# Performance work log

Hardware: AMD Instinct MI355X
Metric: run time of the kernel (lower is better)

The kernel has to match this reference:

```python
import jax, jax.numpy as jnp
import numpy as np

N = 8192   # number of points
C = 64     # feature channels (in_channels == out_channels in PointTrans_Layer)
K = 16     # KNNGraph(k=16)


def mlp2(h, w1, b1, gamma, beta, w2, b2):
    # PyG MLP(num_layers=2): Linear -> BatchNorm(eval: affine) -> ReLU -> Linear
    h = h @ w1 + b1
    h = gamma * h + beta          # BN in eval mode with running mean 0 / var 1
    h = jax.nn.relu(h)
    return h @ w2 + b2


def knn_indices(pos, k):
    # pairwise squared distances, self excluded (KNNGraph loop=False)
    sq = jnp.sum(pos * pos, axis=-1)                      # [N]
    d = sq[:, None] + sq[None, :] - 2.0 * (pos @ pos.T)   # [N, N]
    n = pos.shape[0]
    d = d.at[jnp.arange(n), jnp.arange(n)].set(jnp.inf)
    _, idx = jax.lax.top_k(-d, k)                         # [N, k] nearest neighbors
    return idx


def setup_inputs() -> dict:
    key = jax.random.key(0)
    ks = jax.random.split(key, 20)
    s = 1.0 / np.sqrt(C)
    inp = {
        "x": jax.random.normal(ks[0], (N, C), jnp.float32),
        "pos": jax.random.uniform(ks[1], (N, 3), jnp.float32) * 10.0,
        # PointTransformerConv linears
        "w_src": jax.random.normal(ks[2], (C, C), jnp.float32) * s,   # lin_src (no bias)
        "w_dst": jax.random.normal(ks[3], (C, C), jnp.float32) * s,   # lin_dst (no bias)
        "w_lin": jax.random.normal(ks[4], (C, C), jnp.float32) * s,   # lin (value)
        "b_lin": jnp.zeros((C,), jnp.float32),
        # pos_nn: MLP(3 -> C -> C)
        "p1w": jax.random.normal(ks[5], (3, C), jnp.float32) * (1.0 / np.sqrt(3)),
        "p1b": jnp.zeros((C,), jnp.float32),
        "p1g": jnp.ones((C,), jnp.float32),
        "p1bt": jnp.zeros((C,), jnp.float32),
        "p2w": jax.random.normal(ks[6], (C, C), jnp.float32) * s,
        "p2b": jnp.zeros((C,), jnp.float32),
        # attn_nn: MLP(C -> C -> C)
        "a1w": jax.random.normal(ks[7], (C, C), jnp.float32) * s,
        "a1b": jnp.zeros((C,), jnp.float32),
        "a1g": jnp.ones((C,), jnp.float32),
        "a1bt": jnp.zeros((C,), jnp.float32),
        "a2w": jax.random.normal(ks[8], (C, C), jnp.float32) * s,
        "a2b": jnp.zeros((C,), jnp.float32),
        # linear_up
        "uw": jax.random.normal(ks[9], (C, C), jnp.float32) * s,
        "ub": jnp.zeros((C,), jnp.float32),
    }
    return inp


def reference(x, pos, w_src, w_dst, w_lin, b_lin,
              p1w, p1b, p1g, p1bt, p2w, p2b,
              a1w, a1b, a1g, a1bt, a2w, a2b, uw, ub):
    idx = knn_indices(pos, K)                       # [N, K] neighbor (source) ids
    a_dst = x @ w_dst                               # alpha_i   [N, C]
    a_src = x @ w_src                               # alpha_j   [N, C]
    v = x @ w_lin + b_lin                           # values    [N, C]

    rel = pos[:, None, :] - pos[idx]                # pos_i - pos_j  [N, K, 3]
    delta = mlp2(rel, p1w, p1b, p1g, p1bt, p2w, p2b)            # [N, K, C]
    alpha = a_dst[:, None, :] - a_src[idx] + delta              # [N, K, C]
    alpha = mlp2(alpha, a1w, a1b, a1g, a1bt, a2w, a2b)          # [N, K, C]
    w = jax.nn.softmax(alpha, axis=1)               # softmax over incoming edges
    out = jnp.sum(w * (v[idx] + delta), axis=1)     # [N, C]

    out = out @ uw + ub                             # linear_up
    return out + x                                  # residual
```

## Files before the change

kernel.cpp:

```cpp
#include <hip/hip_runtime.h>
#include <math.h>

#define N 8192
#define C 64
#define K 16
#define NB 8
#define QB 8
#define LNODES 8
#define HS 72

typedef unsigned long long u64;
typedef unsigned int u32;

typedef float  f32x4v  __attribute__((ext_vector_type(4)));
typedef __bf16 bf16x8  __attribute__((ext_vector_type(8)));

__device__ __forceinline__ unsigned short bfr(float f) {
    u32 u = __float_as_uint(f);
    return (unsigned short)((u + 0x7fffu + ((u >> 16) & 1u)) >> 16);
}

__global__ __launch_bounds__(256) void prep_pos4(const float* __restrict__ pos,
                                                 float4* __restrict__ pos4) {
    int j = blockIdx.x * 256 + threadIdx.x;
    if (j < N) {
        const float px = pos[3*j], py = pos[3*j+1], pz = pos[3*j+2];
        pos4[j] = make_float4(px, py, pz, fmaf(px, px, fmaf(py, py, pz * pz)));
    }
}

__global__ __launch_bounds__(256) void prep_wT(const float* __restrict__ p2w,
                                               const float* __restrict__ a1w,
                                               const float* __restrict__ a2w,
                                               unsigned short* __restrict__ wT) {
    int t = blockIdx.x * 256 + threadIdx.x;
    if (t < 3 * C * C) {
        const int m = t >> 12, r = t & (C*C - 1);
        const int e = r >> 6, c = r & 63;
        const float* w = (m == 0) ? p2w : (m == 1) ? a1w : a2w;
        wT[m * C * HS + c * HS + e] = bfr(w[r]);
    }
}

__global__ __launch_bounds__(512) void knn_kernel(const float4* __restrict__ pos4,
                                                  int* __restrict__ idx_out) {
    __shared__ float          smin[QB][512];
    __shared__ float          sthr[QB];
    __shared__ unsigned short s_tl[QB][64];
    __shared__ int            s_tlc[QB];
    __shared__ int            s_buf[QB][96];
    __shared__ double         s_d[QB][96];
    __shared__ int            s_cnt[QB];
    __shared__ double         s_fd[QB][K];
    __shared__ int            s_fi[QB][K];

    const int tid  = threadIdx.x;
    const int w    = tid >> 6;
    const int lane = tid & 63;
    const int i0   = blockIdx.x * QB;

    if (tid < QB) { s_cnt[tid] = 0; s_tlc[tid] = 0; }

    float qx[QB], qy[QB], qz[QB];
    #pragma unroll
    for (int q = 0; q < QB; ++q) {
        const float4 p = pos4[i0 + q];
        qx[q] = p.x; qy[q] = p.y; qz[q] = p.z;
    }

    float mn[QB];
    #pragma unroll
    for (int q = 0; q < QB; ++q) mn[q] = INFINITY;
    #pragma unroll 4
    for (int s = 0; s < 16; ++s) {
        const int j = (s << 9) + tid;
        const float4 pj = pos4[j];
        #pragma unroll
        for (int q = 0; q < QB; ++q) {
            const float dot = fmaf(qx[q], pj.x, fmaf(qy[q], pj.y, qz[q] * pj.z));
            const float pr  = fmaf(-2.0f, dot, pj.w);
            mn[q] = fminf(mn[q], pr);
        }
    }
    #pragma unroll
    for (int q = 0; q < QB; ++q) smin[q][tid] = mn[q];
    __syncthreads();

    float thw;
    {
        float v[8];
        #pragma unroll
        for (int k = 0; k < 8; ++k) v[k] = smin[w][lane + 64*k];
        float ml = fminf(fminf(fminf(v[0], v[1]), fminf(v[2], v[3])),
                         fminf(fminf(v[4], v[5]), fminf(v[6], v[7])));
        float cur = ml, T = 0.0f;
        for (int r = 0; r < K + 1; ++r) {
            float m = cur;
            #pragma unroll
            for (int off = 32; off; off >>= 1) m = fminf(m, __shfl_xor(m, off, 64));
            T = m;
            cur = (cur == m) ? INFINITY : cur;
        }
        thw = T + 1e-3f + 4e-6f * fabsf(T);
        if (lane == 0) sthr[w] = thw;
        #pragma unroll
        for (int k = 0; k < 8; ++k) {
            if (v[k] <= thw) {
                const int slot = atomicAdd(&s_tlc[w], 1);
                if (slot < 64) s_tl[w][slot] = (unsigned short)(lane + 64*k);
            }
        }
    }

    {
        const int lc_raw = s_tlc[w];
        const int lc = lc_raw < 64 ? lc_raw : 64;
        const float qwx = qx[w], qwy = qy[w], qwz = qz[w];
        for (int p = lane; p < lc * 16; p += 64) {
            const int t = s_tl[w][p >> 4];
            const int s = p & 15;
            const int j = (s << 9) + t;
            const float4 pj = pos4[j];
            const float dot = fmaf(qwx, pj.x, fmaf(qwy, pj.y, qwz * pj.z));
            const float pr  = fmaf(-2.0f, dot, pj.w);
            if (pr <= thw) {
                const int slot = atomicAdd(&s_cnt[w], 1);
                if (slot < 96) s_buf[w][slot] = j;
            }
        }
    }

    {
        const int q  = w;
        const int iq = i0 + q;
        const int cno = s_cnt[q];
        if (cno <= 96 && s_tlc[q] <= 64) {
            const int cn = cno;
            const double dqx = (double)qx[q], dqy = (double)qy[q], dqz = (double)qz[q];
            for (int sl = lane; sl < cn; sl += 64) {
                const int jj = s_buf[q][sl];
                const float4 pj = pos4[jj];
                const double dx = dqx - (double)pj.x;
                const double dy = dqy - (double)pj.y;
                const double dz = dqz - (double)pj.z;
                s_d[q][sl] = dx*dx + dy*dy + dz*dz;
            }
            for (int sl = lane; sl < cn; sl += 64) {
                const int jj = s_buf[q][sl];
                if (jj == iq) continue;
                const double dj = s_d[q][sl];
                int r = 0;
                for (int e = 0; e < cn; ++e) {
                    const double de = s_d[q][e];
                    const int    je = s_buf[q][e];
                    r += (de < dj || (de == dj && je < jj)) ? 1 : 0;
                }
                const int selfb = (dj > 0.0 || (dj == 0.0 && iq < jj)) ? 1 : 0;
                const int rr = r - selfb;
                if (rr < K) idx_out[iq*K + rr] = jj;
            }
        } else {
            if (lane == 0) {
                for (int kk = 0; kk < K; ++kk) { s_fd[w][kk] = 1e300; s_fi[w][kk] = 0x7fffffff; }
                const double dqx = (double)qx[q], dqy = (double)qy[q], dqz = (double)qz[q];
                for (int j = 0; j < N; ++j) {
                    if (j == iq) continue;
                    const float4 pj = pos4[j];
                    const double dx = dqx - (double)pj.x;
                    const double dy = dqy - (double)pj.y;
                    const double dz = dqz - (double)pj.z;
                    const double dd = dx*dx + dy*dy + dz*dz;
                    if (dd < s_fd[w][K-1] || (dd == s_fd[w][K-1] && j < s_fi[w][K-1])) {
                        int p = K - 1;
                        while (p > 0 && (dd < s_fd[w][p-1] || (dd == s_fd[w][p-1] && j < s_fi[w][p-1]))) {
                            s_fd[w][p] = s_fd[w][p-1]; s_fi[w][p] = s_fi[w][p-1]; --p;
                        }
                        s_fd[w][p] = dd; s_fi[w][p] = j;
                    }
                }
                for (int kk = 0; kk < K; ++kk) idx_out[iq*K + kk] = s_fi[w][kk];
            }
        }
    }
}

__global__ __launch_bounds__(192) void lin3_kernel(const float* __restrict__ x,
    const float* __restrict__ w_src, const float* __restrict__ w_dst,
    const float* __restrict__ w_lin, const float* __restrict__ b_lin,
    float* __restrict__ a_dst, float* __restrict__ a_src, float* __restrict__ v) {
    __shared__ float xr[LNODES][C];
    const int n0  = blockIdx.x * LNODES;
    const int tid = threadIdx.x;
    const int cc  = tid & 63;
    const int m   = tid >> 6;

    const float* w = (m == 0) ? w_dst : (m == 1) ? w_src : w_lin;
    float wreg[C];
    #pragma unroll
    for (int k = 0; k < C; ++k) wreg[k] = w[k*C + cc];

    for (int t = tid; t < LNODES*C; t += 192) xr[t >> 6][t & 63] = x[n0*C + t];
    __syncthreads();

    const float binit = (m == 2) ? b_lin[cc] : 0.0f;
    float* o = (m == 0) ? a_dst : (m == 1) ? a_src : v;
    for (int nn = 0; nn < LNODES; ++nn) {
        float acc = binit;
        const float4* xv = (const float4*)xr[nn];
        #pragma unroll
        for (int k4 = 0; k4 < 16; ++k4) {
            const float4 xx = xv[k4];
            acc = fmaf(xx.x, wreg[4*k4+0], acc);
            acc = fmaf(xx.y, wreg[4*k4+1], acc);
            acc = fmaf(xx.z, wreg[4*k4+2], acc);
            acc = fmaf(xx.w, wreg[4*k4+3], acc);
        }
        o[(n0 + nn)*C + cc] = acc;
    }
}

__device__ __forceinline__ void mm16x64(const unsigned short* Hb, const unsigned short* wT,
                                        int c0, int sg, f32x4v acc[4]) {
    const bf16x8 a0 = *reinterpret_cast<const bf16x8*>(Hb + c0*HS + sg*8);
    const bf16x8 a1 = *reinterpret_cast<const bf16x8*>(Hb + c0*HS + 32 + sg*8);
    #pragma unroll
    for (int q = 0; q < 4; ++q) {
        const unsigned short* wr = wT + (q*16 + c0)*HS + sg*8;
        const bf16x8 b0 = *reinterpret_cast<const bf16x8*>(wr);
        const bf16x8 b1 = *reinterpret_cast<const bf16x8*>(wr + 32);
        acc[q] = __builtin_amdgcn_mfma_f32_16x16x32_bf16(a0, b0, acc[q], 0, 0, 0);
        acc[q] = __builtin_amdgcn_mfma_f32_16x16x32_bf16(a1, b1, acc[q], 0, 0, 0);
    }
}

__global__ __launch_bounds__(512, 4) void edge_kernel(
    const float* __restrict__ x, const float* __restrict__ pos,
    const int* __restrict__ nidx,
    const float* __restrict__ a_dst, const float* __restrict__ a_src, const float* __restrict__ v,
    const unsigned short* __restrict__ wTg,
    const float* __restrict__ p1w, const float* __restrict__ p1b,
    const float* __restrict__ p1g, const float* __restrict__ p1bt,
    const float* __restrict__ p2b,
    const float* __restrict__ a1b, const float* __restrict__ a1g, const float* __restrict__ a1bt,
    const float* __restrict__ a2b,
    const float* __restrict__ uw, const float* __restrict__ ub,
    float* __restrict__ out) {

    __shared__ __align__(16) unsigned short sWT[3 * C * HS];
    __shared__ __align__(16) float          uwf[C * C];
    __shared__ __align__(16) unsigned short sHb[NB * K * HS];
    __shared__ __align__(16) float4         sMisc4[NB * 16];
    __shared__ int                          sIdx[NB * K];

    const int tid  = threadIdx.x;
    const int w    = tid >> 6;
    const int lane = tid & 63;
    const int c0   = tid & 15;
    const int sg   = (tid >> 4) & 3;
    const int n    = blockIdx.x * NB + w;

    unsigned short* Hlb = sHb + w * (K * HS);
    float4*         Ml4 = sMisc4 + w * 16;
    float*          Mlf = (float*)Ml4;
    int*            Il  = sIdx + w * K;

    {
        const float4* s4 = (const float4*)wTg;
        float4* d4 = (float4*)sWT;
        #pragma unroll
        for (int q = 0; q < 4; ++q) {
            const int e = tid + q*512;
            if (e < 1728) d4[e] = s4[e];
        }
        float4* du = (float4*)uwf;
        const float4* su = (const float4*)uw;
        du[tid] = su[tid]; du[tid + 512] = su[tid + 512];
    }
    if (lane < K) {
        const int j = nidx[n*K + lane];
        Il[lane] = j;
        float4 r;
        r.x = pos[3*n]   - pos[3*j];
        r.y = pos[3*n+1] - pos[3*j+1];
        r.z = pos[3*n+2] - pos[3*j+2];
        r.w = 0.0f;
        Ml4[lane] = r;
    }
    __syncthreads();

    int c4[4];
    #pragma unroll
    for (int q = 0; q < 4; ++q) c4[q] = q*16 + c0;

    {
        float W0[4], W1[4], W2[4], B_[4], G_[4], BT[4];
        #pragma unroll
        for (int q = 0; q < 4; ++q) {
            const int cc = c4[q];
            W0[q] = p1w[cc]; W1[q] = p1w[C + cc]; W2[q] = p1w[2*C + cc];
            B_[q] = p1b[cc]; G_[q] = p1g[cc];     BT[q] = p1bt[cc];
        }
        #pragma unroll
        for (int r = 0; r < 4; ++r) {
            const float4 rr = Ml4[sg*4 + r];
            #pragma unroll
            for (int q = 0; q < 4; ++q) {
                float t = fmaf(rr.x, W0[q], fmaf(rr.y, W1[q], fmaf(rr.z, W2[q], B_[q])));
                t = fmaxf(fmaf(G_[q], t, BT[q]), 0.0f);
                Hlb[(sg*4 + r)*HS + c4[q]] = bfr(t);
            }
        }
    }

    f32x4v acc[4], del[4];
    #pragma unroll
    for (int q = 0; q < 4; ++q) { const float b_ = p2b[c4[q]]; acc[q] = (f32x4v){b_, b_, b_, b_}; }
    mm16x64(Hlb, sWT, c0, sg, acc);
    #pragma unroll
    for (int q = 0; q < 4; ++q) del[q] = acc[q];

    int jr[4];
    #pragma unroll
    for (int r = 0; r < 4; ++r) jr[r] = Il[sg*4 + r];
    float adstv[4];
    #pragma unroll
    for (int q = 0; q < 4; ++q) adstv[q] = a_dst[n*C + c4[q]];

    #pragma unroll
    for (int r = 0; r < 4; ++r) {
        #pragma unroll
        for (int q = 0; q < 4; ++q) {
            const float t = adstv[q] - a_src[jr[r]*C + c4[q]] + acc[q][r];
            Hlb[(sg*4 + r)*HS + c4[q]] = bfr(t);
        }
    }

    #pragma unroll
    for (int q = 0; q < 4; ++q) { const float b_ = a1b[c4[q]]; acc[q] = (f32x4v){b_, b_, b_, b_}; }
    mm16x64(Hlb, sWT + C*HS, c0, sg, acc);
    #pragma unroll
    for (int q = 0; q < 4; ++q) {
        const float g_ = a1g[c4[q]], bt_ = a1bt[c4[q]];
        #pragma unroll
        for (int r = 0; r < 4; ++r) {
            const float h2 = fmaxf(fmaf(g_, acc[q][r], bt_), 0.0f);
            Hlb[(sg*4 + r)*HS + c4[q]] = bfr(h2);
        }
    }

    #pragma unroll
    for (int q = 0; q < 4; ++q) { const float b_ = a2b[c4[q]]; acc[q] = (f32x4v){b_, b_, b_, b_}; }
    mm16x64(Hlb, sWT + 2*C*HS, c0, sg, acc);

    float o_[4];
    #pragma unroll
    for (int q = 0; q < 4; ++q) {
        float vgq[4];
        #pragma unroll
        for (int r = 0; r < 4; ++r) vgq[r] = v[jr[r]*C + c4[q]];
        float lm = fmaxf(fmaxf(acc[q][0], acc[q][1]), fmaxf(acc[q][2], acc[q][3]));
        lm = fmaxf(lm, __shfl_xor(lm, 16, 64));
        lm = fmaxf(lm, __shfl_xor(lm, 32, 64));
        float ls = 0.0f, lo = 0.0f;
        #pragma unroll
        for (int r = 0; r < 4; ++r) {
            const float e_ = __expf(acc[q][r] - lm);
            ls += e_;
            lo = fmaf(e_, vgq[r] + del[q][r], lo);
        }
        ls += __shfl_xor(ls, 16, 64); ls += __shfl_xor(ls, 32, 64);
        lo += __shfl_xor(lo, 16, 64); lo += __shfl_xor(lo, 32, 64);
        o_[q] = lo / ls;
    }
    if (sg == 0) {
        #pragma unroll
        for (int q = 0; q < 4; ++q) Mlf[c4[q]] = o_[q];
    }

    float facc = ub[lane] + x[n*C + lane];
    #pragma unroll 4
    for (int e4 = 0; e4 < 16; ++e4) {
        const float4 g4 = Ml4[e4];
        facc = fmaf(g4.x, uwf[(e4*4+0)*C + lane], facc);
        facc = fmaf(g4.y, uwf[(e4*4+1)*C + lane], facc);
        facc = fmaf(g4.z, uwf[(e4*4+2)*C + lane], facc);
        facc = fmaf(g4.w, uwf[(e4*4+3)*C + lane], facc);
    }
    out[n*C + lane] = facc;
}

extern "C" void kernel_launch(void* const* d_in, const int* in_sizes, int n_in,
                              void* d_out, int out_size, void* d_ws, size_t ws_size,
                              hipStream_t stream) {
    const float* x     = (const float*)d_in[0];
    const float* pos   = (const float*)d_in[1];
    const float* w_src = (const float*)d_in[2];
    const float* w_dst = (const float*)d_in[3];
    const float* w_lin = (const float*)d_in[4];
    const float* b_lin = (const float*)d_in[5];
    const float* p1w   = (const float*)d_in[6];
    const float* p1b   = (const float*)d_in[7];
    const float* p1g   = (const float*)d_in[8];
    const float* p1bt  = (const float*)d_in[9];
    const float* p2w   = (const float*)d_in[10];
    const float* p2b   = (const float*)d_in[11];
    const float* a1w   = (const float*)d_in[12];
    const float* a1b   = (const float*)d_in[13];
    const float* a1g   = (const float*)d_in[14];
    const float* a1bt  = (const float*)d_in[15];
    const float* a2w   = (const float*)d_in[16];
    const float* a2b   = (const float*)d_in[17];
    const float* uw    = (const float*)d_in[18];
    const float* ub    = (const float*)d_in[19];
    float* out = (float*)d_out;

    char* ws    = (char*)d_ws;
    int*    idx  = (int*)ws;
    float*  adst = (float*)(ws + (size_t)N*K*sizeof(int));
    float*  asrc = adst + (size_t)N*C;
    float*  vv   = asrc + (size_t)N*C;
    float4* pos4 = (float4*)(vv + (size_t)N*C);
    unsigned short* wTg = (unsigned short*)(pos4 + N);

    prep_pos4 <<<(N + 255)/256, 256, 0, stream>>>(pos, pos4);
    prep_wT   <<<(3*C*C + 255)/256, 256, 0, stream>>>(p2w, a1w, a2w, wTg);
    knn_kernel<<<N/QB, 512, 0, stream>>>(pos4, idx);
    lin3_kernel<<<N/LNODES, 192, 0, stream>>>(x, w_src, w_dst, w_lin, b_lin, adst, asrc, vv);
    edge_kernel<<<N/NB, 512, 0, stream>>>(x, pos, idx, adst, asrc, vv, wTg,
        p1w, p1b, p1g, p1bt, p2b, a1b, a1g, a1bt, a2b, uw, ub, out);
}
```

Baseline: 62.88 us.

## Fuse KNN into edge kernel and merge prep kernels into one launch

Merges the two prep kernels into a single launch and fuses the KNN search into the edge kernel. Neighbor indices now stay in shared memory, and the shared-memory areas of the two phases are overlaid with a union. This removes the global idx round trip and two kernel launches. The uw matrix is now read from global memory instead of being staged in LDS, which lowers LDS use and lets occupancy rise to 6 blocks. The cost is that KNN and edge work are serialized inside one block and can no longer overlap the way separate kernels did.

```diff
diff --git a/kernel.cpp b/kernel.cpp
--- a/kernel.cpp
+++ b/kernel.cpp
@@ -20,166 +20,23 @@
     return (unsigned short)((u + 0x7fffu + ((u >> 16) & 1u)) >> 16);
 }
 
-__global__ __launch_bounds__(256) void prep_pos4(const float* __restrict__ pos,
-                                                 float4* __restrict__ pos4) {
-    int j = blockIdx.x * 256 + threadIdx.x;
-    if (j < N) {
-        const float px = pos[3*j], py = pos[3*j+1], pz = pos[3*j+2];
-        pos4[j] = make_float4(px, py, pz, fmaf(px, px, fmaf(py, py, pz * pz)));
-    }
-}
-
-__global__ __launch_bounds__(256) void prep_wT(const float* __restrict__ p2w,
-                                               const float* __restrict__ a1w,
-                                               const float* __restrict__ a2w,
-                                               unsigned short* __restrict__ wT) {
-    int t = blockIdx.x * 256 + threadIdx.x;
-    if (t < 3 * C * C) {
-        const int m = t >> 12, r = t & (C*C - 1);
-        const int e = r >> 6, c = r & 63;
-        const float* w = (m == 0) ? p2w : (m == 1) ? a1w : a2w;
-        wT[m * C * HS + c * HS + e] = bfr(w[r]);
-    }
-}
-
-__global__ __launch_bounds__(512) void knn_kernel(const float4* __restrict__ pos4,
-                                                  int* __restrict__ idx_out) {
-    __shared__ float          smin[QB][512];
-    __shared__ float          sthr[QB];
-    __shared__ unsigned short s_tl[QB][64];
-    __shared__ int            s_tlc[QB];
-    __shared__ int            s_buf[QB][96];
-    __shared__ double         s_d[QB][96];
-    __shared__ int            s_cnt[QB];
-    __shared__ double         s_fd[QB][K];
-    __shared__ int            s_fi[QB][K];
-
-    const int tid  = threadIdx.x;
-    const int w    = tid >> 6;
-    const int lane = tid & 63;
-    const int i0   = blockIdx.x * QB;
-
-    if (tid < QB) { s_cnt[tid] = 0; s_tlc[tid] = 0; }
-
-    float qx[QB], qy[QB], qz[QB];
-    #pragma unroll
-    for (int q = 0; q < QB; ++q) {
-        const float4 p = pos4[i0 + q];
-        qx[q] = p.x; qy[q] = p.y; qz[q] = p.z;
-    }
-
-    float mn[QB];
-    #pragma unroll
-    for (int q = 0; q < QB; ++q) mn[q] = INFINITY;
-    #pragma unroll 4
-    for (int s = 0; s < 16; ++s) {
-        const int j = (s << 9) + tid;
-        const float4 pj = pos4[j];
-        #pragma unroll
-        for (int q = 0; q < QB; ++q) {
-            const float dot = fmaf(qx[q], pj.x, fmaf(qy[q], pj.y, qz[q] * pj.z));
-            const float pr  = fmaf(-2.0f, dot, pj.w);
-            mn[q] = fminf(mn[q], pr);
-        }
-    }
-    #pragma unroll
-    for (int q = 0; q < QB; ++q) smin[q][tid] = mn[q];
-    __syncthreads();
-
-    float thw;
-    {
-        float v[8];
-        #pragma unroll
-        for (int k = 0; k < 8; ++k) v[k] = smin[w][lane + 64*k];
-        float ml = fminf(fminf(fminf(v[0], v[1]), fminf(v[2], v[3])),
-                         fminf(fminf(v[4], v[5]), fminf(v[6], v[7])));
-        float cur = ml, T = 0.0f;
-        for (int r = 0; r < K + 1; ++r) {
-            float m = cur;
-            #pragma unroll
-            for (int off = 32; off; off >>= 1) m = fminf(m, __shfl_xor(m, off, 64));
-            T = m;
-            cur = (cur == m) ? INFINITY : cur;
-        }
-        thw = T + 1e-3f + 4e-6f * fabsf(T);
-        if (lane == 0) sthr[w] = thw;
-        #pragma unroll
-        for (int k = 0; k < 8; ++k) {
-            if (v[k] <= thw) {
-                const int slot = atomicAdd(&s_tlc[w], 1);
-                if (slot < 64) s_tl[w][slot] = (unsigned short)(lane + 64*k);
-            }
-        }
-    }
-
-    {
-        const int lc_raw = s_tlc[w];
-        const int lc = lc_raw < 64 ? lc_raw : 64;
-        const float qwx = qx[w], qwy = qy[w], qwz = qz[w];
-        for (int p = lane; p < lc * 16; p += 64) {
-            const int t = s_tl[w][p >> 4];
-            const int s = p & 15;
-            const int j = (s << 9) + t;
-            const float4 pj = pos4[j];
-            const float dot = fmaf(qwx, pj.x, fmaf(qwy, pj.y, qwz * pj.z));
-            const float pr  = fmaf(-2.0f, dot, pj.w);
-            if (pr <= thw) {
-                const int slot = atomicAdd(&s_cnt[w], 1);
-                if (slot < 96) s_buf[w][slot] = j;
-            }
-        }
-    }
-
-    {
-        const int q  = w;
-        const int iq = i0 + q;
-        const int cno = s_cnt[q];
-        if (cno <= 96 && s_tlc[q] <= 64) {
-            const int cn = cno;
-            const double dqx = (double)qx[q], dqy = (double)qy[q], dqz = (double)qz[q];
-            for (int sl = lane; sl < cn; sl += 64) {
-                const int jj = s_buf[q][sl];
-                const float4 pj = pos4[jj];
-                const double dx = dqx - (double)pj.x;
-                const double dy = dqy - (double)pj.y;
-                const double dz = dqz - (double)pj.z;
-                s_d[q][sl] = dx*dx + dy*dy + dz*dz;
-            }
-            for (int sl = lane; sl < cn; sl += 64) {
-                const int jj = s_buf[q][sl];
-                if (jj == iq) continue;
-                const double dj = s_d[q][sl];
-                int r = 0;
-                for (int e = 0; e < cn; ++e) {
-                    const double de = s_d[q][e];
-                    const int    je = s_buf[q][e];
-                    r += (de < dj || (de == dj && je < jj)) ? 1 : 0;
-                }
-                const int selfb = (dj > 0.0 || (dj == 0.0 && iq < jj)) ? 1 : 0;
-                const int rr = r - selfb;
-                if (rr < K) idx_out[iq*K + rr] = jj;
-            }
-        } else {
-            if (lane == 0) {
-                for (int kk = 0; kk < K; ++kk) { s_fd[w][kk] = 1e300; s_fi[w][kk] = 0x7fffffff; }
-                const double dqx = (double)qx[q], dqy = (double)qy[q], dqz = (double)qz[q];
-                for (int j = 0; j < N; ++j) {
-                    if (j == iq) continue;
-                    const float4 pj = pos4[j];
-                    const double dx = dqx - (double)pj.x;
-                    const double dy = dqy - (double)pj.y;
-                    const double dz = dqz - (double)pj.z;
-                    const double dd = dx*dx + dy*dy + dz*dz;
-                    if (dd < s_fd[w][K-1] || (dd == s_fd[w][K-1] && j < s_fi[w][K-1])) {
-                        int p = K - 1;
-                        while (p > 0 && (dd < s_fd[w][p-1] || (dd == s_fd[w][p-1] && j < s_fi[w][p-1]))) {
-                            s_fd[w][p] = s_fd[w][p-1]; s_fi[w][p] = s_fi[w][p-1]; --p;
-                        }
-                        s_fd[w][p] = dd; s_fi[w][p] = j;
-                    }
-                }
-                for (int kk = 0; kk < K; ++kk) idx_out[iq*K + kk] = s_fi[w][kk];
-            }
+__global__ __launch_bounds__(256) void prep_all(const float* __restrict__ pos,
+                                                float4* __restrict__ pos4,
+                                                const float* __restrict__ p2w,
+                                                const float* __restrict__ a1w,
+                                                const float* __restrict__ a2w,
+                                                unsigned short* __restrict__ wT) {
+    const int id = blockIdx.x * 256 + threadIdx.x;
+    if (id < N) {
+        const float px = pos[3*id], py = pos[3*id+1], pz = pos[3*id+2];
+        pos4[id] = make_float4(px, py, pz, fmaf(px, px, fmaf(py, py, pz * pz)));
+    } else {
+        const int t = id - N;
+        if (t < 3 * C * C) {
+            const int m = t >> 12, r = t & (C*C - 1);
+            const int e = r >> 6, c = r & 63;
+            const float* w = (m == 0) ? p2w : (m == 1) ? a1w : a2w;
+            wT[m * C * HS + c * HS + e] = bfr(w[r]);
         }
     }
 }
@@ -233,9 +90,25 @@
     }
 }
 
-__global__ __launch_bounds__(512, 4) void edge_kernel(
-    const float* __restrict__ x, const float* __restrict__ pos,
-    const int* __restrict__ nidx,
+struct __align__(16) KnnSh {
+    float          smin[QB][512];
+    double         s_d[QB][96];
+    double         s_fd[QB][K];
+    int            s_buf[QB][96];
+    int            s_fi[QB][K];
+    unsigned short s_tl[QB][64];
+    int            s_cnt[QB];
+    int            s_tlc[QB];
+};
+struct __align__(16) EdgeSh {
+    unsigned short sWT[3 * C * HS];
+    unsigned short sHb[NB * K * HS];
+    float4         sMisc4[NB * 16];
+};
+
+__global__ __launch_bounds__(512, 6) void knn_edge_kernel(
+    const float4* __restrict__ pos4,
+    const float* __restrict__ x,
     const float* __restrict__ a_dst, const float* __restrict__ a_src, const float* __restrict__ v,
     const unsigned short* __restrict__ wTg,
     const float* __restrict__ p1w, const float* __restrict__ p1b,
@@ -246,45 +119,162 @@
     const float* __restrict__ uw, const float* __restrict__ ub,
     float* __restrict__ out) {
 
-    __shared__ __align__(16) unsigned short sWT[3 * C * HS];
-    __shared__ __align__(16) float          uwf[C * C];
-    __shared__ __align__(16) unsigned short sHb[NB * K * HS];
-    __shared__ __align__(16) float4         sMisc4[NB * 16];
-    __shared__ int                          sIdx[NB * K];
+    __shared__ union __align__(16) ShU { KnnSh k; EdgeSh e; } sh;
+    __shared__ int sIdxL[NB * K];
 
     const int tid  = threadIdx.x;
     const int w    = tid >> 6;
     const int lane = tid & 63;
-    const int c0   = tid & 15;
-    const int sg   = (tid >> 4) & 3;
-    const int n    = blockIdx.x * NB + w;
-
-    unsigned short* Hlb = sHb + w * (K * HS);
-    float4*         Ml4 = sMisc4 + w * 16;
-    float*          Mlf = (float*)Ml4;
-    int*            Il  = sIdx + w * K;
+    const int i0   = blockIdx.x * QB;
+
+    if (tid < QB) { sh.k.s_cnt[tid] = 0; sh.k.s_tlc[tid] = 0; }
+
+    float qx[QB], qy[QB], qz[QB];
+    #pragma unroll
+    for (int q = 0; q < QB; ++q) {
+        const float4 p = pos4[i0 + q];
+        qx[q] = p.x; qy[q] = p.y; qz[q] = p.z;
+    }
+
+    {
+        float mn[QB];
+        #pragma unroll
+        for (int q = 0; q < QB; ++q) mn[q] = INFINITY;
+        #pragma unroll 4
+        for (int s = 0; s < 16; ++s) {
+            const int j = (s << 9) + tid;
+            const float4 pj = pos4[j];
+            #pragma unroll
+            for (int q = 0; q < QB; ++q) {
+                const float dot = fmaf(qx[q], pj.x, fmaf(qy[q], pj.y, qz[q] * pj.z));
+                const float pr  = fmaf(-2.0f, dot, pj.w);
+                mn[q] = fminf(mn[q], pr);
+            }
+        }
+        #pragma unroll
+        for (int q = 0; q < QB; ++q) sh.k.smin[q][tid] = mn[q];
+    }
+    __syncthreads();
+
+    float thw;
+    {
+        float vv[8];
+        #pragma unroll
+        for (int k = 0; k < 8; ++k) vv[k] = sh.k.smin[w][lane + 64*k];
+        float ml = fminf(fminf(fminf(vv[0], vv[1]), fminf(vv[2], vv[3])),
+                         fminf(fminf(vv[4], vv[5]), fminf(vv[6], vv[7])));
+        float cur = ml, T = 0.0f;
+        for (int r = 0; r < K + 1; ++r) {
+            float m = cur;
+            #pragma unroll
+            for (int off = 32; off; off >>= 1) m = fminf(m, __shfl_xor(m, off, 64));
+            T = m;
+            cur = (cur == m) ? INFINITY : cur;
+        }
+        thw = T + 1e-3f + 4e-6f * fabsf(T);
+        #pragma unroll
+        for (int k = 0; k < 8; ++k) {
+            if (vv[k] <= thw) {
+                const int slot = atomicAdd(&sh.k.s_tlc[w], 1);
+                if (slot < 64) sh.k.s_tl[w][slot] = (unsigned short)(lane + 64*k);
+            }
+        }
+    }
+
+    {
+        const int lc_raw = sh.k.s_tlc[w];
+        const int lc = lc_raw < 64 ? lc_raw : 64;
+        const float qwx = qx[w], qwy = qy[w], qwz = qz[w];
+        for (int p = lane; p < lc * 16; p += 64) {
+            const int t = sh.k.s_tl[w][p >> 4];
+            const int s = p & 15;
+            const int j = (s << 9) + t;
+            const float4 pj = pos4[j];
+            const float dot = fmaf(qwx, pj.x, fmaf(qwy, pj.y, qwz * pj.z));
+            const float pr  = fmaf(-2.0f, dot, pj.w);
+            if (pr <= thw) {
+                const int slot = atomicAdd(&sh.k.s_cnt[w], 1);
+                if (slot < 96) sh.k.s_buf[w][slot] = j;
+            }
+        }
+    }
+
+    {
+        const int q  = w;
+        const int iq = i0 + q;
+        const int cno = sh.k.s_cnt[q];
+        if (cno <= 96 && sh.k.s_tlc[q] <= 64) {
+            const int cn = cno;
+            const double dqx = (double)qx[q], dqy = (double)qy[q], dqz = (double)qz[q];
+            for (int sl = lane; sl < cn; sl += 64) {
+                const int jj = sh.k.s_buf[q][sl];
+                const float4 pj = pos4[jj];
+                const double dx = dqx - (double)pj.x;
+                const double dy = dqy - (double)pj.y;
+                const double dz = dqz - (double)pj.z;
+                sh.k.s_d[q][sl] = dx*dx + dy*dy + dz*dz;
+            }
+            for (int sl = lane; sl < cn; sl += 64) {
+                const int jj = sh.k.s_buf[q][sl];
+                if (jj == iq) continue;
+                const double dj = sh.k.s_d[q][sl];
+                int r = 0;
+                for (int e = 0; e < cn; ++e) {
+                    const double de = sh.k.s_d[q][e];
+                    const int    je = sh.k.s_buf[q][e];
+                    r += (de < dj || (de == dj && je < jj)) ? 1 : 0;
+                }
+                const int selfb = (dj > 0.0 || (dj == 0.0 && iq < jj)) ? 1 : 0;
+                const int rr = r - selfb;
+                if (rr < K) sIdxL[q*K + rr] = jj;
+            }
+        } else {
+            if (lane == 0) {
+                for (int kk = 0; kk < K; ++kk) { sh.k.s_fd[w][kk] = 1e300; sh.k.s_fi[w][kk] = 0x7fffffff; }
+                const double dqx = (double)qx[q], dqy = (double)qy[q], dqz = (double)qz[q];
+                for (int j = 0; j < N; ++j) {
+                    if (j == iq) continue;
+                    const float4 pj = pos4[j];
+                    const double dx = dqx - (double)pj.x;
+                    const double dy = dqy - (double)pj.y;
+                    const double dz = dqz - (double)pj.z;
+                    const double dd = dx*dx + dy*dy + dz*dz;
+                    if (dd < sh.k.s_fd[w][K-1] || (dd == sh.k.s_fd[w][K-1] && j < sh.k.s_fi[w][K-1])) {
+                        int p = K - 1;
+                        while (p > 0 && (dd < sh.k.s_fd[w][p-1] || (dd == sh.k.s_fd[w][p-1] && j < sh.k.s_fi[w][p-1]))) {
+                            sh.k.s_fd[w][p] = sh.k.s_fd[w][p-1]; sh.k.s_fi[w][p] = sh.k.s_fi[w][p-1]; --p;
+                        }
+                        sh.k.s_fd[w][p] = dd; sh.k.s_fi[w][p] = j;
+                    }
+                }
+                for (int kk = 0; kk < K; ++kk) sIdxL[w*K + kk] = sh.k.s_fi[w][kk];
+            }
+        }
+    }
+    __syncthreads();
+
+    const int c0 = tid & 15;
+    const int sg = (tid >> 4) & 3;
+    const int n  = i0 + w;
+
+    unsigned short* Hlb = sh.e.sHb + w * (K * HS);
+    float4*         Ml4 = sh.e.sMisc4 + w * 16;
+    int*            Il  = sIdxL + w * K;
 
     {
         const float4* s4 = (const float4*)wTg;
-        float4* d4 = (float4*)sWT;
+        float4* d4 = (float4*)sh.e.sWT;
         #pragma unroll
         for (int q = 0; q < 4; ++q) {
             const int e = tid + q*512;
             if (e < 1728) d4[e] = s4[e];
         }
-        float4* du = (float4*)uwf;
-        const float4* su = (const float4*)uw;
-        du[tid] = su[tid]; du[tid + 512] = su[tid + 512];
     }
     if (lane < K) {
-        const int j = nidx[n*K + lane];
-        Il[lane] = j;
-        float4 r;
-        r.x = pos[3*n]   - pos[3*j];
-        r.y = pos[3*n+1] - pos[3*j+1];
-        r.z = pos[3*n+2] - pos[3*j+2];
-        r.w = 0.0f;
-        Ml4[lane] = r;
+        const int j = Il[lane];
+        const float4 pn = pos4[n];
+        const float4 pj = pos4[j];
+        Ml4[lane] = make_float4(pn.x - pj.x, pn.y - pj.y, pn.z - pj.z, 0.0f);
     }
     __syncthreads();
 
@@ -315,7 +305,7 @@
     f32x4v acc[4], del[4];
     #pragma unroll
     for (int q = 0; q < 4; ++q) { const float b_ = p2b[c4[q]]; acc[q] = (f32x4v){b_, b_, b_, b_}; }
-    mm16x64(Hlb, sWT, c0, sg, acc);
+    mm16x64(Hlb, sh.e.sWT, c0, sg, acc);
     #pragma unroll
     for (int q = 0; q < 4; ++q) del[q] = acc[q];
 
@@ -337,7 +327,7 @@
 
     #pragma unroll
     for (int q = 0; q < 4; ++q) { const float b_ = a1b[c4[q]]; acc[q] = (f32x4v){b_, b_, b_, b_}; }
-    mm16x64(Hlb, sWT + C*HS, c0, sg, acc);
+    mm16x64(Hlb, sh.e.sWT + C*HS, c0, sg, acc);
     #pragma unroll
     for (int q = 0; q < 4; ++q) {
         const float g_ = a1g[c4[q]], bt_ = a1bt[c4[q]];
@@ -350,7 +340,7 @@
 
     #pragma unroll
     for (int q = 0; q < 4; ++q) { const float b_ = a2b[c4[q]]; acc[q] = (f32x4v){b_, b_, b_, b_}; }
-    mm16x64(Hlb, sWT + 2*C*HS, c0, sg, acc);
+    mm16x64(Hlb, sh.e.sWT + 2*C*HS, c0, sg, acc);
 
     float o_[4];
     #pragma unroll
@@ -372,6 +362,7 @@
         lo += __shfl_xor(lo, 16, 64); lo += __shfl_xor(lo, 32, 64);
         o_[q] = lo / ls;
     }
+    float* Mlf = (float*)Ml4;
     if (sg == 0) {
         #pragma unroll
         for (int q = 0; q < 4; ++q) Mlf[c4[q]] = o_[q];
@@ -381,10 +372,10 @@
     #pragma unroll 4
     for (int e4 = 0; e4 < 16; ++e4) {
         const float4 g4 = Ml4[e4];
-        facc = fmaf(g4.x, uwf[(e4*4+0)*C + lane], facc);
-        facc = fmaf(g4.y, uwf[(e4*4+1)*C + lane], facc);
-        facc = fmaf(g4.z, uwf[(e4*4+2)*C + lane], facc);
-        facc = fmaf(g4.w, uwf[(e4*4+3)*C + lane], facc);
+        facc = fmaf(g4.x, uw[(e4*4+0)*C + lane], facc);
+        facc = fmaf(g4.y, uw[(e4*4+1)*C + lane], facc);
+        facc = fmaf(g4.z, uw[(e4*4+2)*C + lane], facc);
+        facc = fmaf(g4.w, uw[(e4*4+3)*C + lane], facc);
     }
     out[n*C + lane] = facc;
 }
@@ -415,17 +406,14 @@
     float* out = (float*)d_out;
 
     char* ws    = (char*)d_ws;
-    int*    idx  = (int*)ws;
-    float*  adst = (float*)(ws + (size_t)N*K*sizeof(int));
+    float*  adst = (float*)ws;
     float*  asrc = adst + (size_t)N*C;
     float*  vv   = asrc + (size_t)N*C;
     float4* pos4 = (float4*)(vv + (size_t)N*C);
     unsigned short* wTg = (unsigned short*)(pos4 + N);
 
-    prep_pos4 <<<(N + 255)/256, 256, 0, stream>>>(pos, pos4);
-    prep_wT   <<<(3*C*C + 255)/256, 256, 0, stream>>>(p2w, a1w, a2w, wTg);
-    knn_kernel<<<N/QB, 512, 0, stream>>>(pos4, idx);
+    prep_all<<<(N + 3*C*C + 255)/256, 256, 0, stream>>>(pos, pos4, p2w, a1w, a2w, wTg);
     lin3_kernel<<<N/LNODES, 192, 0, stream>>>(x, w_src, w_dst, w_lin, b_lin, adst, asrc, vv);
-    edge_kernel<<<N/NB, 512, 0, stream>>>(x, pos, idx, adst, asrc, vv, wTg,
+    knn_edge_kernel<<<N/QB, 512, 0, stream>>>(pos4, x, adst, asrc, vv, wTg,
         p1w, p1b, p1g, p1bt, p2b, a1b, a1g, a1bt, a2b, uw, ub, out);
 }
```

Result: no change. 63.75 us (+1.4%).

## Shrink edge kernel LDS by streaming weights and merge prep kernels

Applied to the files above, without the earlier changes.

The edge kernel no longer holds all three bf16 weight matrices plus the fp32 up-projection in LDS. It reuses a single 64x72 weight buffer, reloading it from global memory before each MFMA stage behind block barriers, and reads uw directly from global memory. It also raises launch bounds to 8 blocks per CU, reads the precomputed pos4, and merges the two prep kernels into one launch. The smaller LDS footprint targets higher occupancy, at the cost of two extra full-block syncs and repeated weight reloads per block.

```diff
diff --git a/kernel.cpp b/kernel.cpp
--- a/kernel.cpp
+++ b/kernel.cpp
@@ -20,25 +20,24 @@
     return (unsigned short)((u + 0x7fffu + ((u >> 16) & 1u)) >> 16);
 }
 
-__global__ __launch_bounds__(256) void prep_pos4(const float* __restrict__ pos,
-                                                 float4* __restrict__ pos4) {
-    int j = blockIdx.x * 256 + threadIdx.x;
-    if (j < N) {
-        const float px = pos[3*j], py = pos[3*j+1], pz = pos[3*j+2];
-        pos4[j] = make_float4(px, py, pz, fmaf(px, px, fmaf(py, py, pz * pz)));
-    }
-}
-
-__global__ __launch_bounds__(256) void prep_wT(const float* __restrict__ p2w,
-                                               const float* __restrict__ a1w,
-                                               const float* __restrict__ a2w,
-                                               unsigned short* __restrict__ wT) {
-    int t = blockIdx.x * 256 + threadIdx.x;
-    if (t < 3 * C * C) {
-        const int m = t >> 12, r = t & (C*C - 1);
-        const int e = r >> 6, c = r & 63;
-        const float* w = (m == 0) ? p2w : (m == 1) ? a1w : a2w;
-        wT[m * C * HS + c * HS + e] = bfr(w[r]);
+__global__ __launch_bounds__(256) void prep_all(const float* __restrict__ pos,
+                                                float4* __restrict__ pos4,
+                                                const float* __restrict__ p2w,
+                                                const float* __restrict__ a1w,
+                                                const float* __restrict__ a2w,
+                                                unsigned short* __restrict__ wT) {
+    const int id = blockIdx.x * 256 + threadIdx.x;
+    if (id < N) {
+        const float px = pos[3*id], py = pos[3*id+1], pz = pos[3*id+2];
+        pos4[id] = make_float4(px, py, pz, fmaf(px, px, fmaf(py, py, pz * pz)));
+    } else {
+        const int t = id - N;
+        if (t < 3 * C * C) {
+            const int m = t >> 12, r = t & (C*C - 1);
+            const int e = r >> 6, c = r & 63;
+            const float* w = (m == 0) ? p2w : (m == 1) ? a1w : a2w;
+            wT[m * C * HS + c * HS + e] = bfr(w[r]);
+        }
     }
 }
 
@@ -233,8 +232,8 @@
     }
 }
 
-__global__ __launch_bounds__(512, 4) void edge_kernel(
-    const float* __restrict__ x, const float* __restrict__ pos,
+__global__ __launch_bounds__(512, 8) void edge_kernel(
+    const float* __restrict__ x, const float4* __restrict__ pos4,
     const int* __restrict__ nidx,
     const float* __restrict__ a_dst, const float* __restrict__ a_src, const float* __restrict__ v,
     const unsigned short* __restrict__ wTg,
@@ -246,8 +245,7 @@
     const float* __restrict__ uw, const float* __restrict__ ub,
     float* __restrict__ out) {
 
-    __shared__ __align__(16) unsigned short sWT[3 * C * HS];
-    __shared__ __align__(16) float          uwf[C * C];
+    __shared__ __align__(16) unsigned short wbuf[C * HS];
     __shared__ __align__(16) unsigned short sHb[NB * K * HS];
     __shared__ __align__(16) float4         sMisc4[NB * 16];
     __shared__ int                          sIdx[NB * K];
@@ -261,30 +259,20 @@
 
     unsigned short* Hlb = sHb + w * (K * HS);
     float4*         Ml4 = sMisc4 + w * 16;
-    float*          Mlf = (float*)Ml4;
     int*            Il  = sIdx + w * K;
 
     {
         const float4* s4 = (const float4*)wTg;
-        float4* d4 = (float4*)sWT;
-        #pragma unroll
-        for (int q = 0; q < 4; ++q) {
-            const int e = tid + q*512;
-            if (e < 1728) d4[e] = s4[e];
-        }
-        float4* du = (float4*)uwf;
-        const float4* su = (const float4*)uw;
-        du[tid] = su[tid]; du[tid + 512] = su[tid + 512];
+        float4* d4 = (float4*)wbuf;
+        d4[tid] = s4[tid];
+        if (tid < 64) d4[tid + 512] = s4[tid + 512];
     }
     if (lane < K) {
         const int j = nidx[n*K + lane];
         Il[lane] = j;
-        float4 r;
-        r.x = pos[3*n]   - pos[3*j];
-        r.y = pos[3*n+1] - pos[3*j+1];
-        r.z = pos[3*n+2] - pos[3*j+2];
-        r.w = 0.0f;
-        Ml4[lane] = r;
+        const float4 pn = pos4[n];
+        const float4 pj = pos4[j];
+        Ml4[lane] = make_float4(pn.x - pj.x, pn.y - pj.y, pn.z - pj.z, 0.0f);
     }
     __syncthreads();
 
@@ -315,7 +303,7 @@
     f32x4v acc[4], del[4];
     #pragma unroll
     for (int q = 0; q < 4; ++q) { const float b_ = p2b[c4[q]]; acc[q] = (f32x4v){b_, b_, b_, b_}; }
-    mm16x64(Hlb, sWT, c0, sg, acc);
+    mm16x64(Hlb, wbuf, c0, sg, acc);
     #pragma unroll
     for (int q = 0; q < 4; ++q) del[q] = acc[q];
 
@@ -334,10 +322,18 @@
             Hlb[(sg*4 + r)*HS + c4[q]] = bfr(t);
         }
     }
+    __syncthreads();
+    {
+        const float4* s4 = (const float4*)(wTg) + 576;
+        float4* d4 = (float4*)wbuf;
+        d4[tid] = s4[tid];
+        if (tid < 64) d4[tid + 512] = s4[tid + 512];
+    }
+    __syncthreads();
 
     #pragma unroll
     for (int q = 0; q < 4; ++q) { const float b_ = a1b[c4[q]]; acc[q] = (f32x4v){b_, b_, b_, b_}; }
-    mm16x64(Hlb, sWT + C*HS, c0, sg, acc);
+    mm16x64(Hlb, wbuf, c0, sg, acc);
     #pragma unroll
     for (int q = 0; q < 4; ++q) {
         const float g_ = a1g[c4[q]], bt_ = a1bt[c4[q]];
@@ -347,10 +343,18 @@
             Hlb[(sg*4 + r)*HS + c4[q]] = bfr(h2);
         }
     }
+    __syncthreads();
+    {
+        const float4* s4 = (const float4*)(wTg) + 1152;
+        float4* d4 = (float4*)wbuf;
+        d4[tid] = s4[tid];
+        if (tid < 64) d4[tid + 512] = s4[tid + 512];
+    }
+    __syncthreads();
 
     #pragma unroll
     for (int q = 0; q < 4; ++q) { const float b_ = a2b[c4[q]]; acc[q] = (f32x4v){b_, b_, b_, b_}; }
-    mm16x64(Hlb, sWT + 2*C*HS, c0, sg, acc);
+    mm16x64(Hlb, wbuf, c0, sg, acc);
 
     float o_[4];
     #pragma unroll
@@ -372,6 +376,7 @@
         lo += __shfl_xor(lo, 16, 64); lo += __shfl_xor(lo, 32, 64);
         o_[q] = lo / ls;
     }
+    float* Mlf = (float*)Ml4;
     if (sg == 0) {
         #pragma unroll
         for (int q = 0; q < 4; ++q) Mlf[c4[q]] = o_[q];
@@ -381,10 +386,10 @@
     #pragma unroll 4
     for (int e4 = 0; e4 < 16; ++e4) {
         const float4 g4 = Ml4[e4];
-        facc = fmaf(g4.x, uwf[(e4*4+0)*C + lane], facc);
-        facc = fmaf(g4.y, uwf[(e4*4+1)*C + lane], facc);
-        facc = fmaf(g4.z, uwf[(e4*4+2)*C + lane], facc);
-        facc = fmaf(g4.w, uwf[(e4*4+3)*C + lane], facc);
+        facc = fmaf(g4.x, uw[(e4*4+0)*C + lane], facc);
+        facc = fmaf(g4.y, uw[(e4*4+1)*C + lane], facc);
+        facc = fmaf(g4.z, uw[(e4*4+2)*C + lane], facc);
+        facc = fmaf(g4.w, uw[(e4*4+3)*C + lane], facc);
     }
     out[n*C + lane] = facc;
 }
@@ -422,10 +427,9 @@
     float4* pos4 = (float4*)(vv + (size_t)N*C);
     unsigned short* wTg = (unsigned short*)(pos4 + N);
 
-    prep_pos4 <<<(N + 255)/256, 256, 0, stream>>>(pos, pos4);
-    prep_wT   <<<(3*C*C + 255)/256, 256, 0, stream>>>(p2w, a1w, a2w, wTg);
+    prep_all<<<(N + 3*C*C + 255)/256, 256, 0, stream>>>(pos, pos4, p2w, a1w, a2w, wTg);
     knn_kernel<<<N/QB, 512, 0, stream>>>(pos4, idx);
     lin3_kernel<<<N/LNODES, 192, 0, stream>>>(x, w_src, w_dst, w_lin, b_lin, adst, asrc, vv);
-    edge_kernel<<<N/NB, 512, 0, stream>>>(x, pos, idx, adst, asrc, vv, wTg,
+    edge_kernel<<<N/NB, 512, 0, stream>>>(x, pos4, idx, adst, asrc, vv, wTg,
         p1w, p1b, p1g, p1bt, p2b, a1b, a1g, a1bt, a2b, uw, ub, out);
 }
```

New measurement: 65.95 us. 1.05x slower.
